# Performance work log

Hardware: AMD Instinct MI355X
Metric: run time of the kernel (lower is better)

The kernel has to match this reference:

```python
import jax, jax.numpy as jnp
import numpy as np

ETA_C = 0.95
ETA_D = 0.95
N_AGENTS = 262144
T = 24
N_NODES = 276  # sum_{t=1}^{23} t


def _build_W():
    # Fixed sparse weight of the 'sum_layer': row j (for slot t, source i) sums
    # pi_c_eta[i] + pi_g[i] + sum_{k=i}^{t-1} pi_s_eta[k]
    W = np.zeros((N_NODES, 3 * T), dtype=np.float32)
    j = 0
    for t in range(1, T):
        for i in range(t):
            W[j, i + 24] = 1.0
            W[j, i + 48] = 1.0
            W[j, i:t] = 1.0
            j += 1
    return W


def _build_idx_mask():
    # idx[t, i] = position in X1 of edge (source i -> slot t); mask marks valid i < t (t >= 1)
    idx = np.zeros((T, T), dtype=np.int32)
    mask = np.zeros((T, T), dtype=bool)
    for t in range(1, T):
        for i in range(t):
            idx[t, i] = t * (t - 1) // 2 + i
            mask[t, i] = True
    return idx, mask

_IDX, _MASK = _build_idx_mask()


def setup_inputs() -> dict:
    key = jax.random.key(0)
    k1, k2, k3 = jax.random.split(key, 3)
    pi_s = jax.random.normal(k1, (N_AGENTS, T), dtype=jnp.float32)
    pi_c = jax.random.normal(k2, (N_AGENTS, T), dtype=jnp.float32)
    pi_g = jax.random.normal(k3, (N_AGENTS, T), dtype=jnp.float32)
    W = jnp.asarray(_build_W())
    return {"pi_s": pi_s, "pi_c": pi_c, "pi_g": pi_g, "W": W, "B": 8}


def reference(pi_s, pi_c, pi_g, W, B):
    idx = jnp.asarray(_IDX)
    mask = jnp.asarray(_MASK)
    # X = [pi_s/eta_d, pi_c/(eta_c*eta_d), pi_g]  -> [N, 72]
    X = jnp.concatenate([pi_s / ETA_D, pi_c / (ETA_C * ETA_D), pi_g], axis=1)
    X1 = X @ W.T  # [N, 276]
    # Gather triangular windows into padded [N, 24, 24]; entry (t, i) valid iff i < t
    Eg = X1[:, idx]
    E = jnp.where(mask, Eg, jnp.inf)
    # X2[:, t] = min_i e_t (row 0 has no sources -> +inf, matching original)
    X2 = jnp.min(E, axis=2)
    # X3[:, t, :t] = softmin(B * e_t); invalid entries exactly 0, row 0 all 0
    NEG = jnp.float32(-1e30)
    logits = jnp.where(mask, -B * Eg, NEG)
    X3 = jax.nn.softmax(logits, axis=2) * mask
    return X2, X3
```

## Files before the change

kernel.cpp:

```cpp
#include <hip/hip_runtime.h>
#include <hip/hip_bf16.h>
#include <math.h>
#include <float.h>

#define T_N 24
#define BLK 256
#define AGS 48

typedef unsigned int u32;
typedef u32 u32x4 __attribute__((ext_vector_type(4)));

__device__ __forceinline__ float decode_B(const void* p) {
    const u32* w = reinterpret_cast<const u32*>(p);
    u32 lo = w[0];
    if (lo != 0u && lo < 0x01000000u) return (float)(int)lo;
    if (lo == 0u) {
        u32 hi = w[1];
        if (hi == 0u) return 0.0f;
        unsigned long long bits = ((unsigned long long)hi << 32);
        return (float)__longlong_as_double((long long)bits);
    }
    return __int_as_float((int)lo);
}

__device__ __forceinline__ u32 f2bf(float f) {
    u32 x = __float_as_uint(f);
    x += 0x7FFFu + ((x >> 16) & 1u);
    return x >> 16;
}

__device__ __forceinline__ float fast_exp2(float x) {
#if defined(__has_builtin) && __has_builtin(__builtin_amdgcn_exp2f)
    return __builtin_amdgcn_exp2f(x);
#else
    return exp2f(x);
#endif
}
__device__ __forceinline__ float fast_log2(float x) {
#if defined(__has_builtin) && __has_builtin(__builtin_amdgcn_logf)
    return __builtin_amdgcn_logf(x);
#else
    return log2f(x);
#endif
}

__device__ __forceinline__ u32 pk_bf16(float lo, float hi) {
    __hip_bfloat162 h = __float22bfloat162_rn(make_float2(lo, hi));
    union { __hip_bfloat162 h2; u32 w; } cv;
    cv.h2 = h;
    return cv.w;
}

__global__ __launch_bounds__(BLK) void ladder_v14_kernel(
    const float* __restrict__ pi_s,
    const float* __restrict__ pi_c,
    const float* __restrict__ pi_g,
    const void* __restrict__ Braw,
    unsigned short* __restrict__ x2_out,
    unsigned short* __restrict__ x3_out,
    int N)
{
    __shared__ float lds[BLK * AGS];

    const float lam = decode_B(Braw) * 1.44269504088896340736f;
    const float inv_cd = 1.0f / (0.95f * 0.95f);
    const float inv_d  = 1.0f / 0.95f;

    const int tid = threadIdx.x;
    const int a0  = blockIdx.x * BLK;
    const int n   = a0 + tid;

    if (n < N) {
        const float4* ps = reinterpret_cast<const float4*>(pi_s + (size_t)n * T_N);
        const float4* pc = reinterpret_cast<const float4*>(pi_c + (size_t)n * T_N);
        const float4* pg = reinterpret_cast<const float4*>(pi_g + (size_t)n * T_N);

        float S = 0.0f, m = FLT_MAX, D = 0.0f;
        float x2prev = 0.0f;
        u32 w[12];
        float4* l4 = reinterpret_cast<float4*>(&lds[tid * AGS]);

        #pragma unroll
        for (int k = 0; k < 6; ++k) {
            float4 vs = ps[k];
            float4 vc = pc[k];
            float4 vg = pg[k];
            float sv[4] = {vs.x, vs.y, vs.z, vs.w};
            float cv[4] = {vc.x, vc.y, vc.z, vc.w};
            float gv[4] = {vg.x, vg.y, vg.z, vg.w};
            float bu4[4], cc4[4];
            #pragma unroll
            for (int j = 0; j < 4; ++j) {
                const int t = 4 * k + j;
                float x2v = (t == 0) ? 0.0f : (S + m);
                if (t & 1) w[t >> 1] = ((t == 1) ? 0x7F7Fu : f2bf(x2prev)) | (f2bf(x2v) << 16);
                else       x2prev = x2v;
                cc4[j] = fmaf(lam, m, -fast_log2(D));
                float u = fmaf(cv[j], inv_cd, gv[j]) - S;
                bu4[j] = lam * u;
                float mn = fminf(m, u);
                D = fmaf(D, fast_exp2(lam * (mn - m)), fast_exp2(lam * (mn - u)));
                m = mn;
                S = fmaf(sv[j], inv_d, S);
            }
            l4[k]     = make_float4(bu4[0], bu4[1], bu4[2], bu4[3]);
            l4[6 + k] = make_float4(cc4[0], cc4[1], cc4[2], cc4[3]);
        }
        uint4* po = reinterpret_cast<uint4*>(x2_out + (size_t)n * T_N);
        #pragma unroll
        for (int q = 0; q < 3; ++q)
            po[q] = make_uint4(w[4*q], w[4*q+1], w[4*q+2], w[4*q+3]);
    }

    __syncthreads();

    const int nbv = N - a0;
    const int nb = (nbv < BLK) ? nbv : BLK;
    if (nb <= 0) return;

    if (nb == BLK) {
        u32x4* p3 = reinterpret_cast<u32x4*>(x3_out + (size_t)a0 * (T_N * T_N));
        int a   = tid / 72;
        int r   = tid - 72 * a;
        int cch = tid;
        #pragma unroll 4
        for (int it = 0; it < 72; ++it) {
            const int t  = (r * 86) >> 8;
            const int i0 = (r - 3 * t) << 3;
            const float* pb = &lds[a * AGS];
            float4 b0 = *reinterpret_cast<const float4*>(pb + i0);
            float4 b1 = *reinterpret_cast<const float4*>(pb + i0 + 4);
            const float ct = pb[T_N + t];
            float bb[8] = {b0.x, b0.y, b0.z, b0.w, b1.x, b1.y, b1.z, b1.w};
            u32 wo[4];
            #pragma unroll
            for (int q = 0; q < 4; ++q) {
                const int ia = i0 + 2 * q, ib = ia + 1;
                float va = fast_exp2((ia < t) ? (ct - bb[2*q])     : -1e30f);
                float vb = fast_exp2((ib < t) ? (ct - bb[2*q + 1]) : -1e30f);
                wo[q] = pk_bf16(va, vb);
            }
            u32x4 v = {wo[0], wo[1], wo[2], wo[3]};
            __builtin_nontemporal_store(v, &p3[cch]);
            cch += BLK;
            r += 40;
            const int cf = (r >= 72);
            a += 3 + cf;
            r -= cf ? 72 : 0;
        }
    } else {
        uint4* p3 = reinterpret_cast<uint4*>(x3_out + (size_t)a0 * (T_N * T_N));
        const int total = nb * 72;
        for (int it = 0; it < 72; ++it) {
            const int cch = it * BLK + tid;
            if (cch >= total) break;
            const u32 cc2 = (u32)cch;
            const u32 a  = cc2 / 72u;
            const u32 r  = cc2 - a * 72u;
            const u32 t  = r / 3u;
            const u32 i0 = (r - t * 3u) * 8u;
            uint4 outv = make_uint4(0u, 0u, 0u, 0u);
            if (i0 < t) {
                const float* pb = &lds[a * AGS];
                float4 b0 = *reinterpret_cast<const float4*>(pb + i0);
                float4 b1 = *reinterpret_cast<const float4*>(pb + i0 + 4);
                const float ct = pb[T_N + t];
                float bb[8] = {b0.x, b0.y, b0.z, b0.w, b1.x, b1.y, b1.z, b1.w};
                u32 wo[4];
                #pragma unroll
                for (int q = 0; q < 4; ++q) {
                    const u32 ia = i0 + 2 * q, ib = ia + 1;
                    float va = fast_exp2((ia < t) ? (ct - bb[2*q])     : -1e30f);
                    float vb = fast_exp2((ib < t) ? (ct - bb[2*q + 1]) : -1e30f);
                    wo[q] = pk_bf16(va, vb);
                }
                outv = make_uint4(wo[0], wo[1], wo[2], wo[3]);
            }
            p3[cch] = outv;
        }
    }
}

extern "C" void kernel_launch(void* const* d_in, const int* in_sizes, int n_in,
                              void* d_out, int out_size, void* d_ws, size_t ws_size,
                              hipStream_t stream) {
    const float* pi_s = (const float*)d_in[0];
    const float* pi_c = (const float*)d_in[1];
    const float* pi_g = (const float*)d_in[2];
    const void* Braw = d_in[4];

    const int N = in_sizes[0] / T_N;
    unsigned short* x2 = (unsigned short*)d_out;
    unsigned short* x3 = x2 + (size_t)N * T_N;

    const int grid = (N + BLK - 1) / BLK;

    hipLaunchKernelGGL(ladder_v14_kernel, dim3(grid), dim3(BLK), 0,
                       stream, pi_s, pi_c, pi_g, Braw, x2, x3, N);
}
```

Baseline: 73.56 us.

## Split fused kernel into params pass and grid-stride softmin streaming pass

When enough workspace is available, the single fused kernel is replaced by two launches. The first computes per-agent scan parameters and X2 and writes the parameters to global workspace. The second is a persistent grid-stride kernel that streams the X3 bf16 output from those parameters. This drops the 48KB LDS buffer and the block barrier, which should raise occupancy for the store-bound phase. In exchange it adds an extra global round trip of about 50MB of parameters, a second launch, and per-chunk integer divisions.

```diff
diff --git a/kernel.cpp b/kernel.cpp
--- a/kernel.cpp
+++ b/kernel.cpp
@@ -51,7 +51,99 @@
     return cv.w;
 }
 
-__global__ __launch_bounds__(BLK) void ladder_v14_kernel(
+
+__global__ __launch_bounds__(BLK) void params_kernel(
+    const float* __restrict__ pi_s,
+    const float* __restrict__ pi_c,
+    const float* __restrict__ pi_g,
+    const void* __restrict__ Braw,
+    unsigned short* __restrict__ x2_out,
+    float* __restrict__ params,
+    int N)
+{
+    const float lam = decode_B(Braw) * 1.44269504088896340736f;
+    const float inv_cd = 1.0f / (0.95f * 0.95f);
+    const float inv_d  = 1.0f / 0.95f;
+
+    const int n = blockIdx.x * blockDim.x + threadIdx.x;
+    if (n >= N) return;
+
+    const float4* ps = reinterpret_cast<const float4*>(pi_s + (size_t)n * T_N);
+    const float4* pc = reinterpret_cast<const float4*>(pi_c + (size_t)n * T_N);
+    const float4* pg = reinterpret_cast<const float4*>(pi_g + (size_t)n * T_N);
+
+    float S = 0.0f, m = FLT_MAX, D = 0.0f;
+    float x2prev = 0.0f;
+    u32 w[12];
+    float4* pp = reinterpret_cast<float4*>(params + (size_t)n * 48);
+
+    #pragma unroll
+    for (int k = 0; k < 6; ++k) {
+        float4 vs = ps[k];
+        float4 vc = pc[k];
+        float4 vg = pg[k];
+        float sv[4] = {vs.x, vs.y, vs.z, vs.w};
+        float cv[4] = {vc.x, vc.y, vc.z, vc.w};
+        float gv[4] = {vg.x, vg.y, vg.z, vg.w};
+        float bu4[4], cc4[4];
+        #pragma unroll
+        for (int j = 0; j < 4; ++j) {
+            const int t = 4 * k + j;
+            float x2v = (t == 0) ? 0.0f : (S + m);
+            if (t & 1) w[t >> 1] = ((t == 1) ? 0x7F7Fu : f2bf(x2prev)) | (f2bf(x2v) << 16);
+            else       x2prev = x2v;
+            cc4[j] = fmaf(lam, m, -fast_log2(D));
+            float u = fmaf(cv[j], inv_cd, gv[j]) - S;
+            bu4[j] = lam * u;
+            float mn = fminf(m, u);
+            D = fmaf(D, fast_exp2(lam * (mn - m)), fast_exp2(lam * (mn - u)));
+            m = mn;
+            S = fmaf(sv[j], inv_d, S);
+        }
+        pp[k]     = make_float4(bu4[0], bu4[1], bu4[2], bu4[3]);
+        pp[6 + k] = make_float4(cc4[0], cc4[1], cc4[2], cc4[3]);
+    }
+    uint4* po = reinterpret_cast<uint4*>(x2_out + (size_t)n * T_N);
+    #pragma unroll
+    for (int q = 0; q < 3; ++q)
+        po[q] = make_uint4(w[4*q], w[4*q+1], w[4*q+2], w[4*q+3]);
+}
+
+__global__ __launch_bounds__(BLK) void stream_kernel(
+    const float* __restrict__ params,
+    unsigned short* __restrict__ x3_out,
+    int total_chunks)
+{
+    int gid = blockIdx.x * blockDim.x + threadIdx.x;
+    const int stride = gridDim.x * blockDim.x;
+    u32x4* p3 = reinterpret_cast<u32x4*>(x3_out);
+
+    for (int cch = gid; cch < total_chunks; cch += stride) {
+        const u32 cc = (u32)cch;
+        const u32 a  = cc / 72u;
+        const u32 r  = cc - 72u * a;
+        const u32 t  = r / 3u;
+        const u32 i0 = (r - 3u * t) * 8u;
+
+        const float* pb = params + (size_t)a * 48u;
+        float4 b0 = *reinterpret_cast<const float4*>(pb + i0);
+        float4 b1 = *reinterpret_cast<const float4*>(pb + i0 + 4);
+        const float ct = pb[24 + t];
+        float bb[8] = {b0.x, b0.y, b0.z, b0.w, b1.x, b1.y, b1.z, b1.w};
+        u32 wo[4];
+        #pragma unroll
+        for (int q = 0; q < 4; ++q) {
+            const u32 ia = i0 + 2 * q, ib = ia + 1;
+            float va = fast_exp2((ia < t) ? (ct - bb[2*q])     : -1e30f);
+            float vb = fast_exp2((ib < t) ? (ct - bb[2*q + 1]) : -1e30f);
+            wo[q] = pk_bf16(va, vb);
+        }
+        u32x4 v = {wo[0], wo[1], wo[2], wo[3]};
+        __builtin_nontemporal_store(v, &p3[cch]);
+    }
+}
+
+__global__ __launch_bounds__(BLK) void ladder_v15_kernel(
     const float* __restrict__ pi_s,
     const float* __restrict__ pi_c,
     const float* __restrict__ pi_g,
@@ -61,11 +153,9 @@
     int N)
 {
     __shared__ float lds[BLK * AGS];
-
     const float lam = decode_B(Braw) * 1.44269504088896340736f;
     const float inv_cd = 1.0f / (0.95f * 0.95f);
     const float inv_d  = 1.0f / 0.95f;
-
     const int tid = threadIdx.x;
     const int a0  = blockIdx.x * BLK;
     const int n   = a0 + tid;
@@ -74,17 +164,13 @@
         const float4* ps = reinterpret_cast<const float4*>(pi_s + (size_t)n * T_N);
         const float4* pc = reinterpret_cast<const float4*>(pi_c + (size_t)n * T_N);
         const float4* pg = reinterpret_cast<const float4*>(pi_g + (size_t)n * T_N);
-
         float S = 0.0f, m = FLT_MAX, D = 0.0f;
         float x2prev = 0.0f;
         u32 w[12];
         float4* l4 = reinterpret_cast<float4*>(&lds[tid * AGS]);
-
         #pragma unroll
         for (int k = 0; k < 6; ++k) {
-            float4 vs = ps[k];
-            float4 vc = pc[k];
-            float4 vg = pg[k];
+            float4 vs = ps[k]; float4 vc = pc[k]; float4 vg = pg[k];
             float sv[4] = {vs.x, vs.y, vs.z, vs.w};
             float cv[4] = {vc.x, vc.y, vc.z, vc.w};
             float gv[4] = {vg.x, vg.y, vg.z, vg.w};
@@ -111,18 +197,13 @@
         for (int q = 0; q < 3; ++q)
             po[q] = make_uint4(w[4*q], w[4*q+1], w[4*q+2], w[4*q+3]);
     }
-
     __syncthreads();
-
     const int nbv = N - a0;
     const int nb = (nbv < BLK) ? nbv : BLK;
     if (nb <= 0) return;
-
     if (nb == BLK) {
         u32x4* p3 = reinterpret_cast<u32x4*>(x3_out + (size_t)a0 * (T_N * T_N));
-        int a   = tid / 72;
-        int r   = tid - 72 * a;
-        int cch = tid;
+        int a = tid / 72, r = tid - 72 * (tid / 72), cch = tid;
         #pragma unroll 4
         for (int it = 0; it < 72; ++it) {
             const int t  = (r * 86) >> 8;
@@ -193,8 +274,20 @@
     unsigned short* x2 = (unsigned short*)d_out;
     unsigned short* x3 = x2 + (size_t)N * T_N;
 
-    const int grid = (N + BLK - 1) / BLK;
-
-    hipLaunchKernelGGL(ladder_v14_kernel, dim3(grid), dim3(BLK), 0,
-                       stream, pi_s, pi_c, pi_g, Braw, x2, x3, N);
-}
+    const size_t need = (size_t)N * 48 * sizeof(float);
+
+    if (ws_size >= need) {
+        float* params = (float*)d_ws;
+        const int gridA = (N + BLK - 1) / BLK;
+        hipLaunchKernelGGL(params_kernel, dim3(gridA), dim3(BLK), 0, stream,
+                           pi_s, pi_c, pi_g, Braw, x2, params, N);
+        const int total_chunks = N * 72;
+        const int gridB = 2048;
+        hipLaunchKernelGGL(stream_kernel, dim3(gridB), dim3(BLK), 0, stream,
+                           params, x3, total_chunks);
+    } else {
+        const int grid = (N + BLK - 1) / BLK;
+        hipLaunchKernelGGL(ladder_v15_kernel, dim3(grid), dim3(BLK), 0,
+                           stream, pi_s, pi_c, pi_g, Braw, x2, x3, N);
+    }
+}
```

After: 100.9 us. 37.1% more time.
